# Kernel optimization log

Hardware: AMD Instinct MI355X
Metric: run time of the kernel (lower is better)

The kernel has to match this reference:

```python
import jax, jax.numpy as jnp
import numpy as np

N = 50000          # nodes
E = 640000         # edges (before self-loops)
DIM_FEATS = 128
DIM_H = 32
HEADS1 = 8
NUM_CLASS = 16
NEG_SLOPE_ATT = 0.2   # PyG GATv2Conv default negative_slope
NEG_SLOPE_OUT = 0.01  # F.leaky_relu default


def setup_inputs() -> dict:
    key = jax.random.key(0)
    ks = jax.random.split(key, 12)
    s = 0.1
    x = jax.random.normal(ks[0], (N, DIM_FEATS), dtype=jnp.float32)
    edge_index = jax.random.randint(ks[1], (2, E), 0, N, dtype=jnp.int32)
    # GATv2Conv layer 1: dim_feats -> dim_h per head, 8 heads, concat
    W1l = jax.random.normal(ks[2], (DIM_FEATS, HEADS1 * DIM_H), dtype=jnp.float32) * s
    W1r = jax.random.normal(ks[3], (DIM_FEATS, HEADS1 * DIM_H), dtype=jnp.float32) * s
    att1 = jax.random.normal(ks[4], (HEADS1, DIM_H), dtype=jnp.float32) * s
    b1 = jnp.zeros((HEADS1 * DIM_H,), dtype=jnp.float32)
    # GATv2Conv layer 2: 256 -> num_class, 1 head, concat=False
    W2l = jax.random.normal(ks[5], (HEADS1 * DIM_H, NUM_CLASS), dtype=jnp.float32) * s
    W2r = jax.random.normal(ks[6], (HEADS1 * DIM_H, NUM_CLASS), dtype=jnp.float32) * s
    att2 = jax.random.normal(ks[7], (1, NUM_CLASS), dtype=jnp.float32) * s
    b2 = jnp.zeros((NUM_CLASS,), dtype=jnp.float32)
    return {"x": x, "edge_index": edge_index, "W1l": W1l, "W1r": W1r,
            "att1": att1, "b1": b1, "W2l": W2l, "W2r": W2r,
            "att2": att2, "b2": b2}


def _segment_softmax(scores, seg, num_segments):
    # scores: [E, H], seg: [E] destination node ids
    m = jax.ops.segment_max(scores, seg, num_segments=num_segments)  # [N, H]
    e = jnp.exp(scores - m[seg])
    denom = jax.ops.segment_sum(e, seg, num_segments=num_segments)   # [N, H]
    return e / (denom[seg] + 1e-16)


def _gatv2_layer(x, src, dst, Wl, Wr, att, bias, heads, out_ch, concat):
    n = x.shape[0]
    xl = (x @ Wl).reshape(n, heads, out_ch)  # source transform
    xr = (x @ Wr).reshape(n, heads, out_ch)  # target transform
    # per-edge GATv2 score: a^T LeakyReLU(xl[j] + xr[i])
    e = jax.nn.leaky_relu(xl[src] + xr[dst], negative_slope=NEG_SLOPE_ATT)  # [E,H,F]
    alpha = jnp.einsum('ehf,hf->eh', e, att)                                # [E,H]
    alpha = _segment_softmax(alpha, dst, n)
    msg = xl[src] * alpha[:, :, None]                                       # [E,H,F]
    out = jax.ops.segment_sum(msg, dst, num_segments=n)                     # [N,H,F]
    out = out.reshape(n, heads * out_ch) if concat else out.mean(axis=1)
    return out + bias


def reference(x, edge_index, W1l, W1r, att1, b1, W2l, W2r, att2, b2):
    # add_self_loops=True (PyG GATv2Conv default)
    loop = jnp.arange(N, dtype=edge_index.dtype)
    src = jnp.concatenate([edge_index[0], loop])
    dst = jnp.concatenate([edge_index[1], loop])
    # eval mode: all dropouts are identity
    h = _gatv2_layer(x, src, dst, W1l, W1r, att1, b1, HEADS1, DIM_H, concat=True)
    h = jax.nn.elu(h)
    h = _gatv2_layer(h, src, dst, W2l, W2r, att2, b2, 1, NUM_CLASS, concat=False)
    return jax.nn.leaky_relu(h, negative_slope=NEG_SLOPE_OUT)
```

## Files before the change

### kernel.cpp

```cpp
#include <hip/hip_runtime.h>
#include <math.h>

#define NN 50000
#define E0 640000
#define ET 690000
#define F1 128
#define D1 256
#define C2 16
#define NB 196
#define MPAD 50048
#define PADK 136
#define LOG2E 1.4426950408889634f
#define NBK1 782

typedef _Float16 f16x8 __attribute__((ext_vector_type(8)));
typedef _Float16 h2 __attribute__((ext_vector_type(2)));
typedef __attribute__((ext_vector_type(4))) float f32x4;

__device__ __forceinline__ unsigned short f2h(float f) {
  union { _Float16 h; unsigned short u; } c;
  c.h = (_Float16)f;
  return c.u;
}
__device__ __forceinline__ float h2f(unsigned short u) {
  union { unsigned short u; _Float16 h; } c; c.u = u; return (float)c.h;
}
__device__ __forceinline__ h2 u2h2(unsigned u) {
  union { unsigned u; h2 h; } c; c.u = u; return c.h;
}
__device__ __forceinline__ unsigned h22u(h2 h) {
  union { h2 h; unsigned u; } c; c.h = h; return c.u;
}

template <int CTRL>
__device__ __forceinline__ float dpp_add(float c) {
  int t = __builtin_amdgcn_update_dpp(0, __builtin_bit_cast(int, c), CTRL, 0xF, 0xF, true);
  return c + __builtin_bit_cast(float, t);
}

__global__ __launch_bounds__(256) void k_prep(
    const float* __restrict__ Wl, const float* __restrict__ Wr,
    const float* __restrict__ W2l, const float* __restrict__ W2r,
    const int* __restrict__ ei,
    unsigned short* __restrict__ wt, unsigned short* __restrict__ wt2,
    int* __restrict__ deg) {
  const int b = blockIdx.x;
  if (b < 256) {
    int tid = b * 256 + threadIdx.x;
    int n = tid >> 7, k = tid & 127;
    float v = (n < 256) ? Wl[k * 256 + n] : Wr[k * 256 + (n - 256)];
    wt[tid] = f2h(v);
  } else if (b < 288) {
    int tid = (b - 256) * 256 + threadIdx.x;
    int n = tid >> 8, k = tid & 255;
    float v = (n < 16) ? W2l[k * 16 + n] : W2r[k * 16 + (n - 16)];
    wt2[tid] = f2h(v);
  } else {
    int e = (b - 288) * 256 + threadIdx.x;
    if (e >= ET) return;
    int d = (e < E0) ? ei[E0 + e] : (e - E0);
    atomicAdd(&deg[d], 1);
  }
}

__global__ __launch_bounds__(256) void k_gemm1m(
    const float* __restrict__ x, const unsigned short* __restrict__ wt,
    unsigned short* __restrict__ xlh, unsigned short* __restrict__ xrh) {
  __shared__ unsigned short Al[64 * PADK];
  __shared__ unsigned short Bl[128 * PADK];
  const int t = threadIdx.x;
  const int m0 = blockIdx.x * 64;
  {
    const int r = t >> 4;
    const int c = (t & 15) * 8;
#pragma unroll
    for (int p = 0; p < 4; ++p) {
      const int row = r + p * 16;
      const int rg = m0 + row;
      const float* xp = &x[(size_t)(rg < NN ? rg : NN - 1) * F1 + c];
      float4 lo = *(const float4*)xp;
      float4 hi = *(const float4*)(xp + 4);
      h2 q0 = h2{(_Float16)lo.x, (_Float16)lo.y};
      h2 q1 = h2{(_Float16)lo.z, (_Float16)lo.w};
      h2 q2 = h2{(_Float16)hi.x, (_Float16)hi.y};
      h2 q3 = h2{(_Float16)hi.z, (_Float16)hi.w};
      uint4 st; st.x = h22u(q0); st.y = h22u(q1); st.z = h22u(q2); st.w = h22u(q3);
      *(uint4*)&Al[row * PADK + c] = st;
    }
  }
  const int wave = t >> 6, lane = t & 63;
  const int mw = (wave >> 1) * 32, nw = (wave & 1) * 64;
  const int fr = lane & 15, fq = lane >> 4;
  for (int ny = 0; ny < 4; ++ny) {
    const int n0 = ny * 128;
    {
      const int r = t >> 4;
      const int c = (t & 15) * 8;
#pragma unroll
      for (int p = 0; p < 8; ++p) {
        const int row = r + p * 16;
        *(float4*)&Bl[row * PADK + c] = *(const float4*)&wt[(size_t)(n0 + row) * F1 + c];
      }
    }
    __syncthreads();
    f32x4 acc[2][4] = {};
#pragma unroll
    for (int ks = 0; ks < 4; ++ks) {
      const int ko = ks * 32 + fq * 8;
      f16x8 a[2], b[4];
#pragma unroll
      for (int i = 0; i < 2; ++i)
        a[i] = *(const f16x8*)&Al[(mw + i * 16 + fr) * PADK + ko];
#pragma unroll
      for (int j = 0; j < 4; ++j)
        b[j] = *(const f16x8*)&Bl[(nw + j * 16 + fr) * PADK + ko];
#pragma unroll
      for (int i = 0; i < 2; ++i)
#pragma unroll
        for (int j = 0; j < 4; ++j)
          acc[i][j] = __builtin_amdgcn_mfma_f32_16x16x32_f16(a[i], b[j], acc[i][j], 0, 0, 0);
    }
    __syncthreads();
    unsigned short* outp = (n0 < 256) ? xlh : xrh;
    const int cb = (n0 & 255) + nw + fr;
#pragma unroll
    for (int j = 0; j < 4; ++j) {
      const int col = cb + j * 16;
      const int head = col >> 5, f = col & 31;
      unsigned short* hp = outp + (size_t)head * NN * 32 + f;
#pragma unroll
      for (int i = 0; i < 2; ++i) {
        const int gm0 = m0 + mw + i * 16 + fq * 4;
#pragma unroll
        for (int r = 0; r < 4; ++r) {
          const int gm = gm0 + r;
          if (gm < NN) hp[(size_t)gm * 32] = f2h(acc[i][j][r]);
        }
      }
    }
  }
}

__global__ __launch_bounds__(256) void k_scan_part(const int* __restrict__ deg,
                                                   int* __restrict__ part) {
  int i = blockIdx.x * 256 + threadIdx.x;
  int v = (i < NN) ? deg[i] : 0;
  v += __shfl_xor(v, 1);  v += __shfl_xor(v, 2);  v += __shfl_xor(v, 4);
  v += __shfl_xor(v, 8);  v += __shfl_xor(v, 16); v += __shfl_xor(v, 32);
  __shared__ int w[4];
  if ((threadIdx.x & 63) == 0) w[threadIdx.x >> 6] = v;
  __syncthreads();
  if (threadIdx.x == 0) part[blockIdx.x] = w[0] + w[1] + w[2] + w[3];
}

__global__ __launch_bounds__(256) void k_scan_apply(int* __restrict__ deg,
                                                    const int* __restrict__ part,
                                                    int* __restrict__ offs) {
  __shared__ int lds[256];
  __shared__ int red[4];
  const int b = blockIdx.x, t = threadIdx.x;
  const int i = b * 256 + t;
  int v = (i < NN) ? deg[i] : 0;
  lds[t] = v;
  int pp = 0;
  for (int j = t; j < b; j += 256) pp += part[j];
  pp += __shfl_xor(pp, 1);  pp += __shfl_xor(pp, 2);  pp += __shfl_xor(pp, 4);
  pp += __shfl_xor(pp, 8);  pp += __shfl_xor(pp, 16); pp += __shfl_xor(pp, 32);
  if ((t & 63) == 0) red[t >> 6] = pp;
  __syncthreads();
  const int prefix = red[0] + red[1] + red[2] + red[3];
  for (int off = 1; off < 256; off <<= 1) {
    int u = (t >= off) ? lds[t - off] : 0;
    __syncthreads();
    lds[t] += u;
    __syncthreads();
  }
  int excl = prefix + lds[t] - v;
  if (i < NN) { offs[i] = excl; deg[i] = excl; }
  if (b == NB - 1 && t == 255) offs[NN] = prefix + lds[255];
}

__global__ void k_scatter(const int* __restrict__ ei, int* __restrict__ cur,
                          unsigned short* __restrict__ csr) {
  int e = blockIdx.x * 256 + threadIdx.x;
  if (e >= ET) return;
  int s, d;
  if (e < E0) { s = ei[e]; d = ei[E0 + e]; } else { s = d = e - E0; }
  int pos = atomicAdd(&cur[d], 1);
  csr[pos] = (unsigned short)s;
}

__global__ __launch_bounds__(256) void k_agg1(
    const unsigned short* __restrict__ xlh, const unsigned short* __restrict__ xrh,
    unsigned short* __restrict__ hb,
    const int* __restrict__ offs, const unsigned short* __restrict__ csr,
    const float* __restrict__ att, const float* __restrict__ b1) {
  const int b = blockIdx.x;
  const int head = b & 7;
  const int wave = threadIdx.x >> 6;
  const int lane = threadIdx.x & 63;
  const int g = lane >> 2;
  const int j4 = lane & 3;
  const int idxn = (b >> 3) * 64 + wave * 16 + g;
  const bool valid = idxn < NN;
  const int n = valid ? idxn : 0;
  const int colh = j4 * 8;
  const int col = head * 32 + colh;
  const unsigned short* xlhead = xlh + (size_t)head * NN * 32;

  const uint4 xru = *(const uint4*)&xrh[((size_t)head * NN + n) * 32 + colh];
  h2 xr2[4];
  xr2[0] = u2h2(xru.x); xr2[1] = u2h2(xru.y);
  xr2[2] = u2h2(xru.z); xr2[3] = u2h2(xru.w);
  float at8[8];
  *(float4*)&at8[0] = *(const float4*)&att[col];
  *(float4*)&at8[4] = *(const float4*)&att[col + 4];
  h2 ath6[4], ath4[4];
#pragma unroll
  for (int j = 0; j < 4; ++j) {
    ath6[j] = h2{(_Float16)(at8[2 * j] * (0.6f * LOG2E)),
                 (_Float16)(at8[2 * j + 1] * (0.6f * LOG2E))};
    ath4[j] = h2{(_Float16)(at8[2 * j] * (0.4f * LOG2E)),
                 (_Float16)(at8[2 * j + 1] * (0.4f * LOG2E))};
  }
  float l = 0.f;
  h2 acc2[4] = {h2{0, 0}, h2{0, 0}, h2{0, 0}, h2{0, 0}};
  const int beg = valid ? offs[n] : 0;
  const int fin = valid ? offs[n + 1] : 0;

  auto XL = [&](int s) -> uint4 {
    return *(const uint4*)&xlhead[(size_t)s * 32 + colh];
  };
  auto edge = [&](const uint4& w) {
    h2 xh[4];
    xh[0] = u2h2(w.x); xh[1] = u2h2(w.y); xh[2] = u2h2(w.z); xh[3] = u2h2(w.w);
    float cv = 0.f, ca = 0.f;
#pragma unroll
    for (int j = 0; j < 4; ++j) {
      h2 v = xh[j] + xr2[j];
      h2 a = u2h2(h22u(v) & 0x7FFF7FFFu);
      cv = __builtin_amdgcn_fdot2(v, ath6[j], cv, false);
      ca = __builtin_amdgcn_fdot2(a, ath4[j], ca, false);
    }
    float c = cv + ca;
    c = dpp_add<0xB1>(c);
    c = dpp_add<0x4E>(c);
    const float p = exp2f(c);
    l += p;
    const _Float16 ph = (_Float16)p;
    const h2 p2 = h2{ph, ph};
#pragma unroll
    for (int j = 0; j < 4; ++j) acc2[j] += p2 * xh[j];
  };

  int idx = beg;
  if (idx + 3 < fin) {
    int s0 = csr[idx], s1 = csr[idx + 1], s2 = csr[idx + 2], s3 = csr[idx + 3];
    uint4 w0 = XL(s0), w1 = XL(s1), w2 = XL(s2), w3 = XL(s3);
    for (;;) {
      const int nx = idx + 4;
      const bool more = nx + 3 < fin;
      const int b0 = more ? nx : beg;
      const int b1i = more ? nx + 1 : beg;
      const int b2i = more ? nx + 2 : beg;
      const int b3i = more ? nx + 3 : beg;
      const int t0 = csr[b0], t1 = csr[b1i], t2 = csr[b2i], t3 = csr[b3i];
      const uint4 v0 = XL(t0), v1 = XL(t1), v2 = XL(t2), v3 = XL(t3);
      edge(w0); edge(w1); edge(w2); edge(w3);
      idx = nx;
      if (!more) break;
      w0 = v0; w1 = v1; w2 = v2; w3 = v3;
    }
  }
  for (; idx < fin; ++idx) {
    const int s = csr[idx];
    const uint4 w = XL(s);
    edge(w);
  }

  if (valid) {
    const float rl = 1.f / (l + 1e-16f);
    float b8[8], o[8];
    *(float4*)&b8[0] = *(const float4*)&b1[col];
    *(float4*)&b8[4] = *(const float4*)&b1[col + 4];
#pragma unroll
    for (int j = 0; j < 4; ++j) {
      o[2 * j]     = (float)acc2[j][0] * rl + b8[2 * j];
      o[2 * j + 1] = (float)acc2[j][1] * rl + b8[2 * j + 1];
    }
#pragma unroll
    for (int k = 0; k < 8; ++k) o[k] = o[k] > 0.f ? o[k] : expm1f(o[k]);
    ushort4 p;
    p.x = f2h(o[0]); p.y = f2h(o[1]); p.z = f2h(o[2]); p.w = f2h(o[3]);
    ushort4 q;
    q.x = f2h(o[4]); q.y = f2h(o[5]); q.z = f2h(o[6]); q.w = f2h(o[7]);
    uint4 packed;
    packed.x = *(unsigned*)&p.x; packed.y = *(unsigned*)&p.z;
    packed.z = *(unsigned*)&q.x; packed.w = *(unsigned*)&q.z;
    *(uint4*)&hb[(size_t)n * D1 + col] = packed;
  }
}

__global__ __launch_bounds__(256) void k_gemm2m(
    const unsigned short* __restrict__ hb, const unsigned short* __restrict__ wt2,
    unsigned short* __restrict__ h2lh, float* __restrict__ h2r) {
  const int t = threadIdx.x;
  const int wave = t >> 6, lane = t & 63;
  const int fr = lane & 15, fq = lane >> 4;
  const int m0 = blockIdx.x * 128 + wave * 32;
  f32x4 acc[2][2] = {};
#pragma unroll
  for (int ks = 0; ks < 8; ++ks) {
    const int ko = ks * 32 + fq * 8;
    f16x8 a[2], b[2];
#pragma unroll
    for (int i = 0; i < 2; ++i) {
      int row = m0 + i * 16 + fr; if (row >= NN) row = NN - 1;
      a[i] = *(const f16x8*)&hb[(size_t)row * D1 + ko];
    }
#pragma unroll
    for (int j = 0; j < 2; ++j)
      b[j] = *(const f16x8*)&wt2[(j * 16 + fr) * 256 + ko];
#pragma unroll
    for (int i = 0; i < 2; ++i)
#pragma unroll
      for (int j = 0; j < 2; ++j)
        acc[i][j] = __builtin_amdgcn_mfma_f32_16x16x32_f16(a[i], b[j], acc[i][j], 0, 0, 0);
  }
#pragma unroll
  for (int i = 0; i < 2; ++i) {
    const int gm0 = m0 + i * 16 + fq * 4;
#pragma unroll
    for (int r = 0; r < 4; ++r) {
      const int gm = gm0 + r;
      if (gm < NN) {
        h2lh[(size_t)gm * C2 + fr] = f2h(acc[i][0][r]);
        h2r[(size_t)gm * C2 + fr] = acc[i][1][r];
      }
    }
  }
}

__global__ __launch_bounds__(256) void k_agg2(
    const unsigned short* __restrict__ h2lh, const float* __restrict__ h2r,
    const int* __restrict__ offs, const unsigned short* __restrict__ csr,
    const float* __restrict__ att2, const float* __restrict__ b2,
    float* __restrict__ out) {
  const int wave = threadIdx.x >> 6;
  const int lane = threadIdx.x & 63;
  const int n = blockIdx.x * 4 + wave;
  if (n >= NN) return;
  const int c = lane & 15, g = lane >> 4;
  const float xr_v = h2r[(size_t)n * C2 + c];
  const float att_v = att2[c] * LOG2E;
  float l = 0.f, acc = 0.f;
  const int beg = offs[n], fin = offs[n + 1];
  for (int idx = beg + g; idx < fin; idx += 8) {
    const int i1 = idx + 4;
    const bool m1 = i1 < fin;
    const int s0 = csr[idx];
    const int s1 = csr[m1 ? i1 : idx];
    const float xl0 = h2f(h2lh[(size_t)s0 * C2 + c]);
    const float xl1 = h2f(h2lh[(size_t)s1 * C2 + c]);
    float v0 = xl0 + xr_v; v0 = fmaxf(v0, 0.2f * v0);
    float v1 = xl1 + xr_v; v1 = fmaxf(v1, 0.2f * v1);
    float sc0 = v0 * att_v, sc1 = v1 * att_v;
    sc0 = dpp_add<0xB1>(sc0);   sc1 = dpp_add<0xB1>(sc1);
    sc0 = dpp_add<0x4E>(sc0);   sc1 = dpp_add<0x4E>(sc1);
    sc0 = dpp_add<0x124>(sc0);  sc1 = dpp_add<0x124>(sc1);
    sc0 = dpp_add<0x128>(sc0);  sc1 = dpp_add<0x128>(sc1);
    const float p0 = exp2f(sc0);
    const float p1 = m1 ? exp2f(sc1) : 0.f;
    l += p0 + p1;
    acc = fmaf(p0, xl0, fmaf(p1, xl1, acc));
  }
  l += __shfl_xor(l, 16);   l += __shfl_xor(l, 32);
  acc += __shfl_xor(acc, 16); acc += __shfl_xor(acc, 32);
  float o = acc / (l + 1e-16f) + b2[c];
  o = o > 0.f ? o : 0.01f * o;
  if (lane < 16) out[(size_t)n * C2 + c] = o;
}

extern "C" void kernel_launch(void* const* d_in, const int* in_sizes, int n_in,
                              void* d_out, int out_size, void* d_ws, size_t ws_size,
                              hipStream_t stream) {
  const float* x    = (const float*)d_in[0];
  const int*   ei   = (const int*)d_in[1];
  const float* W1l  = (const float*)d_in[2];
  const float* W1r  = (const float*)d_in[3];
  const float* att1 = (const float*)d_in[4];
  const float* b1   = (const float*)d_in[5];
  const float* W2l  = (const float*)d_in[6];
  const float* W2r  = (const float*)d_in[7];
  const float* att2 = (const float*)d_in[8];
  const float* b2   = (const float*)d_in[9];
  float* out = (float*)d_out;

  unsigned short* xlh = (unsigned short*)d_ws;
  unsigned short* xrh = xlh + (size_t)NN * D1;
  unsigned short* hb  = xrh + (size_t)NN * D1;
  int* deg  = (int*)(hb + (size_t)NN * D1);
  int* part = deg + NN;
  int* offs = part + NB;
  unsigned short* csr = (unsigned short*)(offs + NN + 1);
  unsigned short* wt  = csr + ET + 2;
  unsigned short* wt2 = wt + 512 * F1;
  unsigned short* h2lh = xlh;
  float* h2r = (float*)(h2lh + (size_t)NN * C2);

  hipMemsetAsync(deg, 0, NN * sizeof(int), stream);
  k_prep<<<288 + (ET + 255) / 256, 256, 0, stream>>>(
      W1l, W1r, W2l, W2r, ei, wt, wt2, deg);
  k_gemm1m<<<MPAD / 64, 256, 0, stream>>>(x, wt, xlh, xrh);
  k_scan_part<<<NB, 256, 0, stream>>>(deg, part);
  k_scan_apply<<<NB, 256, 0, stream>>>(deg, part, offs);
  k_scatter<<<(ET + 255) / 256, 256, 0, stream>>>(ei, deg, csr);
  k_agg1<<<NBK1 * 8, 256, 0, stream>>>(xlh, xrh, hb, offs, csr, att1, b1);
  k_gemm2m<<<(NN + 127) / 128, 256, 0, stream>>>(hb, wt2, h2lh, h2r);
  k_agg2<<<NN / 4, 256, 0, stream>>>(h2lh, h2r, offs, csr, att2, b2, out);
}
```

Before: 259.3 us.

## Load CSR neighbor ids once per lane quad and broadcast via DPP, predicate tail edges

In the layer-1 aggregation, each lane of a 4-lane group now loads one CSR source index and broadcasts it to the others with DPP quad-perm, instead of every lane loading all four indices. The separate scalar tail loop is replaced by predicating the last partial group of four with a live flag that zeroes the probability. The change also swaps the divisions for hardware reciprocal and expm1f for exp2f-1 in the epilogues. This cuts redundant index loads and branch divergence at some cost in wasted work on dummy tail edges and slight precision loss in ELU near zero.

Measured after the change: 256.9 us. About the same (-0.9%).

```diff
diff --git a/kernel.cpp b/kernel.cpp
--- a/kernel.cpp
+++ b/kernel.cpp
@@ -36,6 +36,11 @@
 __device__ __forceinline__ float dpp_add(float c) {
   int t = __builtin_amdgcn_update_dpp(0, __builtin_bit_cast(int, c), CTRL, 0xF, 0xF, true);
   return c + __builtin_bit_cast(float, t);
+}
+template <int K>
+__device__ __forceinline__ int dpp_bcast(int v) {
+  constexpr int ctrl = K | (K << 2) | (K << 4) | (K << 6);
+  return __builtin_amdgcn_update_dpp(0, v, ctrl, 0xF, 0xF, true);
 }
 
 __global__ __launch_bounds__(256) void k_prep(
@@ -228,10 +233,15 @@
   const int beg = valid ? offs[n] : 0;
   const int fin = valid ? offs[n + 1] : 0;
 
-  auto XL = [&](int s) -> uint4 {
+  auto ldids = [&](int base) -> int {
+    int a = base + j4;
+    a = (a < fin) ? a : beg;
+    return (int)csr[a];
+  };
+  auto XLrow = [&](int s) -> uint4 {
     return *(const uint4*)&xlhead[(size_t)s * 32 + colh];
   };
-  auto edge = [&](const uint4& w) {
+  auto edge = [&](const uint4& w, bool live) {
     h2 xh[4];
     xh[0] = u2h2(w.x); xh[1] = u2h2(w.y); xh[2] = u2h2(w.z); xh[3] = u2h2(w.w);
     float cv = 0.f, ca = 0.f;
@@ -245,7 +255,8 @@
     float c = cv + ca;
     c = dpp_add<0xB1>(c);
     c = dpp_add<0x4E>(c);
-    const float p = exp2f(c);
+    float p = exp2f(c);
+    p = live ? p : 0.f;
     l += p;
     const _Float16 ph = (_Float16)p;
     const h2 p2 = h2{ph, ph};
@@ -253,33 +264,27 @@
     for (int j = 0; j < 4; ++j) acc2[j] += p2 * xh[j];
   };
 
-  int idx = beg;
-  if (idx + 3 < fin) {
-    int s0 = csr[idx], s1 = csr[idx + 1], s2 = csr[idx + 2], s3 = csr[idx + 3];
-    uint4 w0 = XL(s0), w1 = XL(s1), w2 = XL(s2), w3 = XL(s3);
-    for (;;) {
-      const int nx = idx + 4;
-      const bool more = nx + 3 < fin;
-      const int b0 = more ? nx : beg;
-      const int b1i = more ? nx + 1 : beg;
-      const int b2i = more ? nx + 2 : beg;
-      const int b3i = more ? nx + 3 : beg;
-      const int t0 = csr[b0], t1 = csr[b1i], t2 = csr[b2i], t3 = csr[b3i];
-      const uint4 v0 = XL(t0), v1 = XL(t1), v2 = XL(t2), v3 = XL(t3);
-      edge(w0); edge(w1); edge(w2); edge(w3);
-      idx = nx;
-      if (!more) break;
-      w0 = v0; w1 = v1; w2 = v2; w3 = v3;
-    }
-  }
-  for (; idx < fin; ++idx) {
-    const int s = csr[idx];
-    const uint4 w = XL(s);
-    edge(w);
+  int ids = ldids(beg);
+  uint4 w0 = XLrow(dpp_bcast<0>(ids));
+  uint4 w1 = XLrow(dpp_bcast<1>(ids));
+  uint4 w2 = XLrow(dpp_bcast<2>(ids));
+  uint4 w3 = XLrow(dpp_bcast<3>(ids));
+  int ids1 = ldids(beg + 4);
+  for (int idx = beg; idx < fin; idx += 4) {
+    const uint4 v0 = XLrow(dpp_bcast<0>(ids1));
+    const uint4 v1 = XLrow(dpp_bcast<1>(ids1));
+    const uint4 v2 = XLrow(dpp_bcast<2>(ids1));
+    const uint4 v3 = XLrow(dpp_bcast<3>(ids1));
+    const int ids2 = ldids(idx + 8);
+    edge(w0, true);
+    edge(w1, idx + 1 < fin);
+    edge(w2, idx + 2 < fin);
+    edge(w3, idx + 3 < fin);
+    w0 = v0; w1 = v1; w2 = v2; w3 = v3; ids1 = ids2;
   }
 
   if (valid) {
-    const float rl = 1.f / (l + 1e-16f);
+    const float rl = __builtin_amdgcn_rcpf(l + 1e-16f);
     float b8[8], o[8];
     *(float4*)&b8[0] = *(const float4*)&b1[col];
     *(float4*)&b8[4] = *(const float4*)&b1[col + 4];
@@ -289,7 +294,8 @@
       o[2 * j + 1] = (float)acc2[j][1] * rl + b8[2 * j + 1];
     }
 #pragma unroll
-    for (int k = 0; k < 8; ++k) o[k] = o[k] > 0.f ? o[k] : expm1f(o[k]);
+    for (int k = 0; k < 8; ++k)
+      o[k] = o[k] > 0.f ? o[k] : exp2f(o[k] * LOG2E) - 1.f;
     ushort4 p;
     p.x = f2h(o[0]); p.y = f2h(o[1]); p.z = f2h(o[2]); p.w = f2h(o[3]);
     ushort4 q;
@@ -376,7 +382,7 @@
   }
   l += __shfl_xor(l, 16);   l += __shfl_xor(l, 32);
   acc += __shfl_xor(acc, 16); acc += __shfl_xor(acc, 32);
-  float o = acc / (l + 1e-16f) + b2[c];
+  float o = acc * __builtin_amdgcn_rcpf(l + 1e-16f) + b2[c];
   o = o > 0.f ? o : 0.01f * o;
   if (lane < 16) out[(size_t)n * C2 + c] = o;
 }
```
